# Optimization experiments

Hardware: AMD Instinct MI355X
Metric: run time of the kernel (lower is better)

## Reference

```python
import jax, jax.numpy as jnp
import numpy as np

HIDDEN = 1024
FFN = 2048
NUM_EXPERTS = 8
TOP_K = 2
BATCH = 1
SEQ = 2048


def setup_inputs() -> dict:
    key = jax.random.key(0)
    ks = jax.random.split(key, 5)
    x = jax.random.normal(ks[0], (BATCH, SEQ, HIDDEN), dtype=jnp.float32)
    gate_w = jax.random.normal(ks[1], (NUM_EXPERTS, HIDDEN), dtype=jnp.float32) * 0.02
    w1 = jax.random.normal(ks[2], (NUM_EXPERTS, FFN, HIDDEN), dtype=jnp.float32) * 0.02
    w3 = jax.random.normal(ks[3], (NUM_EXPERTS, FFN, HIDDEN), dtype=jnp.float32) * 0.02
    w2 = jax.random.normal(ks[4], (NUM_EXPERTS, HIDDEN, FFN), dtype=jnp.float32) * 0.02
    return {"x": x, "gate_w": gate_w, "w1": w1, "w3": w3, "w2": w2}


def reference(x, gate_w, w1, w3, w2):
    B, S, H = x.shape
    tokens = x.reshape(-1, H)                              # [T, H]
    # Router: softmax over expert logits, top-k, renormalize (eval mode: no jitter)
    logits = tokens @ gate_w.T                             # [T, E]
    probs = jax.nn.softmax(logits, axis=-1)
    top_w, top_i = jax.lax.top_k(probs, TOP_K)             # [T, K]
    top_w = top_w / jnp.sum(top_w, axis=-1, keepdims=True)
    # combine[t, e] = routing weight of expert e for token t (0 if not selected)
    combine = jnp.sum(
        jax.nn.one_hot(top_i, NUM_EXPERTS, dtype=tokens.dtype) * top_w[..., None],
        axis=1,
    )                                                      # [T, E]
    out = jnp.zeros_like(tokens)
    for e in range(NUM_EXPERTS):
        h = jax.nn.silu(tokens @ w1[e].T) * (tokens @ w3[e].T)   # [T, F]
        out = out + combine[:, e:e + 1] * (h @ w2[e].T)          # [T, H]
    return out.reshape(B, S, H)
```

## Files before the change

kernel.cpp:

```cpp
#include <hip/hip_runtime.h>
#include <hip/hip_bf16.h>

#define T_TOK 2048
#define HID 1024
#define FFNDIM 2048
#define NEXP 8

typedef __attribute__((ext_vector_type(8))) short short8;
typedef __attribute__((ext_vector_type(4))) float f32x4;

__device__ inline unsigned short f2bf(float f) {
  union { float f; unsigned int u; } v; v.f = f;
  unsigned int u = v.u;
  unsigned int r = (u + 0x7fffu + ((u >> 16) & 1u)) >> 16;
  return (unsigned short)r;
}

__device__ inline short8 pack8(float4 a, float4 b) {
  union { __hip_bfloat162 h2[4]; short8 s; } u;
  u.h2[0] = __float22bfloat162_rn(float2{a.x, a.y});
  u.h2[1] = __float22bfloat162_rn(float2{a.z, a.w});
  u.h2[2] = __float22bfloat162_rn(float2{b.x, b.y});
  u.h2[3] = __float22bfloat162_rn(float2{b.z, b.w});
  return u.s;
}

__device__ inline void gload_lds16(const void* g, void* l) {
  __builtin_amdgcn_global_load_lds((const __attribute__((address_space(1))) void*)g,
                                   (__attribute__((address_space(3))) void*)l, 16, 0, 0);
}

__global__ __launch_bounds__(256) void router_kernel(
    const float* __restrict__ x, const float* __restrict__ gw,
    int* __restrict__ top_i, float* __restrict__ top_w,
    unsigned short* __restrict__ xbf) {
  int lane = threadIdx.x & 63;
  int t = blockIdx.x * 4 + (threadIdx.x >> 6);
  if (t >= T_TOK) return;
  float xv[16];
#pragma unroll
  for (int i = 0; i < 16; ++i) xv[i] = x[(size_t)t * HID + i * 64 + lane];
#pragma unroll
  for (int i = 0; i < 16; ++i) xbf[(size_t)t * HID + i * 64 + lane] = f2bf(xv[i]);
  float logit[NEXP];
#pragma unroll
  for (int e = 0; e < NEXP; ++e) {
    float s = 0.f;
#pragma unroll
    for (int i = 0; i < 16; ++i) s += xv[i] * gw[e * HID + i * 64 + lane];
#pragma unroll
    for (int off = 32; off > 0; off >>= 1) s += __shfl_xor(s, off);
    logit[e] = s;
  }
  if (lane == 0) {
    float mx = logit[0];
#pragma unroll
    for (int e = 1; e < NEXP; ++e) mx = fmaxf(mx, logit[e]);
    float p[NEXP]; float sum = 0.f;
#pragma unroll
    for (int e = 0; e < NEXP; ++e) { p[e] = expf(logit[e] - mx); sum += p[e]; }
#pragma unroll
    for (int e = 0; e < NEXP; ++e) p[e] /= sum;
    int i0 = 0;
#pragma unroll
    for (int e = 1; e < NEXP; ++e) if (p[e] > p[i0]) i0 = e;
    int i1 = (i0 == 0) ? 1 : 0;
#pragma unroll
    for (int e = 0; e < NEXP; ++e) if (e != i0 && p[e] > p[i1]) i1 = e;
    float w0 = p[i0], w1v = p[i1];
    float s2 = w0 + w1v;
    w0 /= s2; w1v /= s2;
    top_i[t * 2 + 0] = i0; top_i[t * 2 + 1] = i1;
    top_w[t * 2 + 0] = w0; top_w[t * 2 + 1] = w1v;
  }
}

__global__ __launch_bounds__(256) void plan_kernel(
    const int* __restrict__ top_i, int* __restrict__ counts,
    int* __restrict__ offsets, int* __restrict__ row_tok,
    int* __restrict__ tok_rows) {
  __shared__ int scnt[NEXP], soff[NEXP], scur[NEXP];
  int tid = threadIdx.x;
  if (tid < NEXP) { scnt[tid] = 0; scur[tid] = 0; }
  __syncthreads();
  for (int i = tid; i < T_TOK * 2; i += 256) atomicAdd(&scnt[top_i[i]], 1);
  __syncthreads();
  if (tid == 0) {
    int s = 0;
    for (int e = 0; e < NEXP; ++e) { soff[e] = s; s += scnt[e]; }
  }
  __syncthreads();
  for (int i = tid; i < T_TOK * 2; i += 256) {
    int e = top_i[i];
    int p = atomicAdd(&scur[e], 1);
    int idx = soff[e] + p;
    row_tok[idx] = i >> 1;
    tok_rows[i] = idx;
  }
  if (tid < NEXP) { counts[tid] = scnt[tid]; offsets[tid] = soff[tid]; }
  if (tid == 0) offsets[NEXP] = T_TOK * 2;
}

__global__ __launch_bounds__(256) void wconv_kernel(
    const float4* __restrict__ s0, const float4* __restrict__ s1,
    const float4* __restrict__ s2,
    short8* __restrict__ d0, short8* __restrict__ d1, short8* __restrict__ d2) {
  const float4* s = (blockIdx.y == 0) ? s0 : (blockIdx.y == 1) ? s1 : s2;
  short8* d = (blockIdx.y == 0) ? d0 : (blockIdx.y == 1) ? d1 : d2;
  const int n8 = NEXP * FFNDIM * HID / 8;
  for (int i = blockIdx.x * 256 + threadIdx.x; i < n8; i += gridDim.x * 256) {
    float4 a = s[2 * i];
    float4 b = s[2 * i + 1];
    d[i] = pack8(a, b);
  }
}

__global__ __launch_bounds__(512, 2) void gemm1_s(
    const unsigned short* __restrict__ xbf, const int* __restrict__ row_tok,
    const unsigned short* __restrict__ Wb1, const unsigned short* __restrict__ Wb3,
    const int* __restrict__ counts, const int* __restrict__ offsets,
    unsigned short* __restrict__ hbuf) {
  constexpr int BK = 64;
  constexpr int ATILE = 128 * BK;
  constexpr int BTILE = 256 * BK;
  extern __shared__ unsigned short sm1[];
  unsigned short* sA = sm1;
  unsigned short* sB = sm1 + 2 * ATILE;

  int e = blockIdx.y;
  int cnt = counts[e];
  int nt = blockIdx.x, mt = blockIdx.z;
  if (cnt == 0 || mt * 128 >= cnt) return;
  int off = offsets[e];
  int ntb = nt * 128;

  int tid = threadIdx.x, lane = tid & 63, wid = tid >> 6;
  int wm = wid >> 2, wn = wid & 3;
  int fr = lane & 15, fq = lane >> 4;

  int ri = tid >> 3;
  int g = tid & 7;
  int gsw = (g ^ (ri & 7)) * 8;

  size_t asrc[2]; int albase[2];
#pragma unroll
  for (int j = 0; j < 2; ++j) {
    int r = j * 64 + ri;
    int rg = mt * 128 + r; if (rg > cnt - 1) rg = cnt - 1;
    int tok = row_tok[off + rg];
    asrc[j] = (size_t)tok * HID + gsw;
    albase[j] = (j * 64 + wid * 8) * BK;
  }
  const unsigned short* bsrc[4]; int blbase[4];
#pragma unroll
  for (int j = 0; j < 4; ++j) {
    int r = j * 64 + ri;
    int wn_ = r >> 6, s = r & 63;
    const unsigned short* mat = (s < 32) ? Wb1 : Wb3;
    bsrc[j] = mat + ((size_t)e * FFNDIM + (ntb + wn_ * 32 + (s & 31))) * HID + gsw;
    blbase[j] = (j * 64 + wid * 8) * BK;
  }

#define STAGE1(P, K0)                                                       \
  do {                                                                      \
    _Pragma("unroll")                                                       \
    for (int j = 0; j < 2; ++j)                                             \
      gload_lds16(xbf + asrc[j] + (K0), &sA[(P) * ATILE + albase[j]]);      \
    _Pragma("unroll")                                                       \
    for (int j = 0; j < 4; ++j)                                             \
      gload_lds16(bsrc[j] + (K0), &sB[(P) * BTILE + blbase[j]]);            \
  } while (0)

  f32x4 acc[4][4];
#pragma unroll
  for (int mf = 0; mf < 4; ++mf)
#pragma unroll
    for (int nf = 0; nf < 4; ++nf) acc[mf][nf] = (f32x4){0.f, 0.f, 0.f, 0.f};

#define COMP1(P)                                                            \
  do {                                                                      \
    _Pragma("unroll")                                                       \
    for (int kk = 0; kk < 2; ++kk) {                                        \
      short8 bfr[4];                                                        \
      _Pragma("unroll")                                                     \
      for (int nf = 0; nf < 4; ++nf) {                                      \
        int R = wn * 64 + nf * 16 + fr;                                     \
        bfr[nf] = *reinterpret_cast<const short8*>(                         \
            &sB[(P) * BTILE + R * BK + (((kk * 4 + fq) ^ (R & 7)) << 3)]);  \
      }                                                                     \
      _Pragma("unroll")                                                     \
      for (int mf = 0; mf < 4; ++mf) {                                      \
        int R = wm * 64 + mf * 16 + fr;                                     \
        short8 afr = *reinterpret_cast<const short8*>(                      \
            &sA[(P) * ATILE + R * BK + (((kk * 4 + fq) ^ (R & 7)) << 3)]);  \
        _Pragma("unroll")                                                   \
        for (int nf = 0; nf < 4; ++nf)                                      \
          acc[mf][nf] = __builtin_amdgcn_mfma_f32_16x16x32_bf16(            \
              afr, bfr[nf], acc[mf][nf], 0, 0, 0);                          \
      }                                                                     \
    }                                                                       \
  } while (0)

  const int NT = HID / BK;
  STAGE1(0, 0);
  __syncthreads();
  int cur = 0;
  for (int t = 0; t < NT; ++t) {
    if (t + 1 < NT) STAGE1(cur ^ 1, (t + 1) * BK);
    COMP1(cur);
    __syncthreads();
    cur ^= 1;
  }

#pragma unroll
  for (int mf = 0; mf < 4; ++mf) {
    int rl = wm * 64 + mf * 16 + fq * 4;
#pragma unroll
    for (int jj = 0; jj < 4; ++jj) {
      int gm = mt * 128 + rl + jj;
      if (gm < cnt) {
#pragma unroll
        for (int nf = 0; nf < 2; ++nf) {
          float h1 = acc[mf][nf][jj];
          float h3 = acc[mf][nf + 2][jj];
          float sv = h1 / (1.f + expf(-h1)) * h3;
          hbuf[(size_t)(off + gm) * FFNDIM + ntb + wn * 32 + nf * 16 + fr] = f2bf(sv);
        }
      }
    }
  }
#undef STAGE1
#undef COMP1
}

__global__ __launch_bounds__(512, 2) void gemm2_p(
    const unsigned short* __restrict__ hbuf, const unsigned short* __restrict__ Wb2,
    const int* __restrict__ counts, const int* __restrict__ offsets,
    float* __restrict__ Yg) {
  constexpr int BK = 64;
  constexpr int ATILE = 256 * BK;
  constexpr int BTILE = 128 * BK;
  extern __shared__ unsigned short sm2[];
  unsigned short* sA = sm2;
  unsigned short* sB = sm2 + 2 * ATILE;

  int zz = blockIdx.y;
  int e = zz & 7, kz = zz >> 3;
  int cnt = counts[e];
  int nt = blockIdx.x, mt = blockIdx.z;
  if (cnt == 0 || mt * 256 >= cnt) return;
  int off = offsets[e];
  int ntb = nt * 128;
  int kbase = kz * (FFNDIM / 2);

  int tid = threadIdx.x, lane = tid & 63, wid = tid >> 6;
  int wm = wid >> 2, wn = wid & 3;
  int fr = lane & 15, fq = lane >> 4;

  int ri = tid >> 3;
  int g = tid & 7;
  int gsw = (g ^ (ri & 7)) * 8;

  size_t asrc[4];
  int albase[4];
#pragma unroll
  for (int j = 0; j < 4; ++j) {
    int r = j * 64 + ri;
    int rg = mt * 256 + r; if (rg > cnt - 1) rg = cnt - 1;
    asrc[j] = (size_t)(off + rg) * FFNDIM + kbase + gsw;
    albase[j] = (j * 64 + wid * 8) * BK;
  }
  const unsigned short* bsrc[2];
  int blbase[2];
#pragma unroll
  for (int j = 0; j < 2; ++j) {
    int r = j * 64 + ri;
    bsrc[j] = Wb2 + ((size_t)e * HID + (ntb + r)) * FFNDIM + kbase + gsw;
    blbase[j] = (j * 64 + wid * 8) * BK;
  }

#define STAGE2(P, K0)                                                       \
  do {                                                                      \
    _Pragma("unroll")                                                       \
    for (int j = 0; j < 4; ++j)                                             \
      gload_lds16(hbuf + asrc[j] + (K0), &sA[(P) * ATILE + albase[j]]);     \
    _Pragma("unroll")                                                       \
    for (int j = 0; j < 2; ++j)                                             \
      gload_lds16(bsrc[j] + (K0), &sB[(P) * BTILE + blbase[j]]);            \
  } while (0)

  f32x4 acc[8][2];
#pragma unroll
  for (int mf = 0; mf < 8; ++mf)
#pragma unroll
    for (int nf = 0; nf < 2; ++nf) acc[mf][nf] = (f32x4){0.f, 0.f, 0.f, 0.f};

#define COMP2(P)                                                            \
  do {                                                                      \
    _Pragma("unroll")                                                       \
    for (int kk = 0; kk < 2; ++kk) {                                        \
      short8 bfr[2];                                                        \
      _Pragma("unroll")                                                     \
      for (int nf = 0; nf < 2; ++nf) {                                      \
        int R = wn * 32 + nf * 16 + fr;                                     \
        bfr[nf] = *reinterpret_cast<const short8*>(                         \
            &sB[(P) * BTILE + R * BK + (((kk * 4 + fq) ^ (R & 7)) << 3)]);  \
      }                                                                     \
      _Pragma("unroll")                                                     \
      for (int mf = 0; mf < 8; ++mf) {                                      \
        int R = wm * 128 + mf * 16 + fr;                                    \
        short8 afr = *reinterpret_cast<const short8*>(                      \
            &sA[(P) * ATILE + R * BK + (((kk * 4 + fq) ^ (R & 7)) << 3)]);  \
        _Pragma("unroll")                                                   \
        for (int nf = 0; nf < 2; ++nf)                                      \
          acc[mf][nf] = __builtin_amdgcn_mfma_f32_16x16x32_bf16(            \
              afr, bfr[nf], acc[mf][nf], 0, 0, 0);                          \
      }                                                                     \
    }                                                                       \
  } while (0)

  const int NT = (FFNDIM / 2) / BK;
  STAGE2(0, 0);
  __syncthreads();
  int cur = 0;
  for (int t = 0; t < NT; ++t) {
    if (t + 1 < NT) STAGE2(cur ^ 1, (t + 1) * BK);
    COMP2(cur);
    __syncthreads();
    cur ^= 1;
  }

  float* yp = Yg + (size_t)kz * (4096 * HID);
#pragma unroll
  for (int mf = 0; mf < 8; ++mf) {
    int rl = wm * 128 + mf * 16 + fq * 4;
#pragma unroll
    for (int jj = 0; jj < 4; ++jj) {
      int gm = mt * 256 + rl + jj;
      if (gm < cnt) {
#pragma unroll
        for (int nf = 0; nf < 2; ++nf)
          yp[(size_t)(off + gm) * HID + ntb + wn * 32 + nf * 16 + fr] = acc[mf][nf][jj];
      }
    }
  }
#undef STAGE2
#undef COMP2
}

__global__ __launch_bounds__(256) void combine_kernel(
    const float* __restrict__ Yg, const int* __restrict__ tok_rows,
    const float* __restrict__ top_w, float* __restrict__ out) {
  int t = blockIdx.x;
  int c = threadIdx.x * 4;
  int r0 = tok_rows[t * 2 + 0];
  int r1 = tok_rows[t * 2 + 1];
  float tw0 = top_w[t * 2 + 0];
  float tw1 = top_w[t * 2 + 1];
  const float* Y0 = Yg;
  const float* Y1 = Yg + (size_t)4096 * HID;
  float4 a0 = *reinterpret_cast<const float4*>(Y0 + (size_t)r0 * HID + c);
  float4 b0 = *reinterpret_cast<const float4*>(Y1 + (size_t)r0 * HID + c);
  float4 a1 = *reinterpret_cast<const float4*>(Y0 + (size_t)r1 * HID + c);
  float4 b1 = *reinterpret_cast<const float4*>(Y1 + (size_t)r1 * HID + c);
  float4 o;
  o.x = tw0 * (a0.x + b0.x) + tw1 * (a1.x + b1.x);
  o.y = tw0 * (a0.y + b0.y) + tw1 * (a1.y + b1.y);
  o.z = tw0 * (a0.z + b0.z) + tw1 * (a1.z + b1.z);
  o.w = tw0 * (a0.w + b0.w) + tw1 * (a1.w + b1.w);
  *reinterpret_cast<float4*>(out + (size_t)t * HID + c) = o;
}

extern "C" void kernel_launch(void* const* d_in, const int* in_sizes, int n_in,
                              void* d_out, int out_size, void* d_ws, size_t ws_size,
                              hipStream_t stream) {
  const float* x  = (const float*)d_in[0];
  const float* gw = (const float*)d_in[1];
  const float* w1 = (const float*)d_in[2];
  const float* w3 = (const float*)d_in[3];
  const float* w2 = (const float*)d_in[4];
  float* out = (float*)d_out;

  char* ws = (char*)d_ws;
  int*   counts   = (int*)(ws + 0);
  int*   offsets  = (int*)(ws + 64);
  int*   top_i    = (int*)(ws + 1024);
  float* top_w    = (float*)(ws + 17408);
  int*   row_tok  = (int*)(ws + 33792);
  int*   tok_rows = (int*)(ws + 50176);
  unsigned short* xbf  = (unsigned short*)(ws + 1048576);
  unsigned short* hbuf = (unsigned short*)(ws + 5242880);
  unsigned short* Wb1  = (unsigned short*)(ws + 22020096);
  unsigned short* Wb3  = (unsigned short*)(ws + 55574528);
  unsigned short* Wb2  = (unsigned short*)(ws + 89128960);
  float*          Yg   = (float*)(ws + 22020096);

  hipFuncSetAttribute((const void*)gemm1_s,
                      hipFuncAttributeMaxDynamicSharedMemorySize, 98304);
  hipFuncSetAttribute((const void*)gemm2_p,
                      hipFuncAttributeMaxDynamicSharedMemorySize, 98304);

  router_kernel<<<T_TOK / 4, 256, 0, stream>>>(x, gw, top_i, top_w, xbf);
  plan_kernel<<<1, 256, 0, stream>>>(top_i, counts, offsets, row_tok, tok_rows);
  wconv_kernel<<<dim3(2048, 3), 256, 0, stream>>>(
      (const float4*)w1, (const float4*)w3, (const float4*)w2,
      (short8*)Wb1, (short8*)Wb3, (short8*)Wb2);

  gemm1_s<<<dim3(16, NEXP, 16), 512, 98304, stream>>>(
      xbf, row_tok, Wb1, Wb3, counts, offsets, hbuf);
  gemm2_p<<<dim3(8, 16, 8), 512, 98304, stream>>>(
      hbuf, Wb2, counts, offsets, Yg);
  combine_kernel<<<T_TOK, 256, 0, stream>>>(Yg, tok_rows, top_w, out);
}
```

Measured before the change: 178.0 us.

## Triple-buffer LDS in both expert GEMMs with raw barriers and partial vmcnt waits

Both expert GEMM kernels move from double-buffered to triple-buffered LDS tiles. Loads are issued two K-steps ahead, and each step waits with a partial s_waitcnt vmcnt plus a raw s_barrier instead of a full __syncthreads, so global-to-LDS copies can overlap compute more deeply. The cost is 144KB of shared memory per block, which drops occupancy from 2 blocks per CU to 1 and changes the launch-bounds hint.

New measurement: 175.2 us. Within noise of the previous version (-1.6%).

```diff
diff --git a/kernel.cpp b/kernel.cpp
--- a/kernel.cpp
+++ b/kernel.cpp
@@ -29,6 +29,9 @@
   __builtin_amdgcn_global_load_lds((const __attribute__((address_space(1))) void*)g,
                                    (__attribute__((address_space(3))) void*)l, 16, 0, 0);
 }
+
+#define RAW_BAR() __builtin_amdgcn_s_barrier()
+#define MEMCLOB() asm volatile("" ::: "memory")
 
 __global__ __launch_bounds__(256) void router_kernel(
     const float* __restrict__ x, const float* __restrict__ gw,
@@ -115,7 +118,7 @@
   }
 }
 
-__global__ __launch_bounds__(512, 2) void gemm1_s(
+__global__ __launch_bounds__(512, 1) void gemm1_r3(
     const unsigned short* __restrict__ xbf, const int* __restrict__ row_tok,
     const unsigned short* __restrict__ Wb1, const unsigned short* __restrict__ Wb3,
     const int* __restrict__ counts, const int* __restrict__ offsets,
@@ -125,7 +128,7 @@
   constexpr int BTILE = 256 * BK;
   extern __shared__ unsigned short sm1[];
   unsigned short* sA = sm1;
-  unsigned short* sB = sm1 + 2 * ATILE;
+  unsigned short* sB = sm1 + 3 * ATILE;
 
   int e = blockIdx.y;
   int cnt = counts[e];
@@ -161,14 +164,14 @@
     blbase[j] = (j * 64 + wid * 8) * BK;
   }
 
-#define STAGE1(P, K0)                                                       \
+#define STAGE1(B, K0)                                                       \
   do {                                                                      \
     _Pragma("unroll")                                                       \
     for (int j = 0; j < 2; ++j)                                             \
-      gload_lds16(xbf + asrc[j] + (K0), &sA[(P) * ATILE + albase[j]]);      \
+      gload_lds16(xbf + asrc[j] + (K0), &sA[(B) * ATILE + albase[j]]);      \
     _Pragma("unroll")                                                       \
     for (int j = 0; j < 4; ++j)                                             \
-      gload_lds16(bsrc[j] + (K0), &sB[(P) * BTILE + blbase[j]]);            \
+      gload_lds16(bsrc[j] + (K0), &sB[(B) * BTILE + blbase[j]]);            \
   } while (0)
 
   f32x4 acc[4][4];
@@ -177,7 +180,7 @@
 #pragma unroll
     for (int nf = 0; nf < 4; ++nf) acc[mf][nf] = (f32x4){0.f, 0.f, 0.f, 0.f};
 
-#define COMP1(P)                                                            \
+#define COMP1(B)                                                            \
   do {                                                                      \
     _Pragma("unroll")                                                       \
     for (int kk = 0; kk < 2; ++kk) {                                        \
@@ -186,13 +189,13 @@
       for (int nf = 0; nf < 4; ++nf) {                                      \
         int R = wn * 64 + nf * 16 + fr;                                     \
         bfr[nf] = *reinterpret_cast<const short8*>(                         \
-            &sB[(P) * BTILE + R * BK + (((kk * 4 + fq) ^ (R & 7)) << 3)]);  \
+            &sB[(B) * BTILE + R * BK + (((kk * 4 + fq) ^ (R & 7)) << 3)]);  \
       }                                                                     \
       _Pragma("unroll")                                                     \
       for (int mf = 0; mf < 4; ++mf) {                                      \
         int R = wm * 64 + mf * 16 + fr;                                     \
         short8 afr = *reinterpret_cast<const short8*>(                      \
-            &sA[(P) * ATILE + R * BK + (((kk * 4 + fq) ^ (R & 7)) << 3)]);  \
+            &sA[(B) * ATILE + R * BK + (((kk * 4 + fq) ^ (R & 7)) << 3)]);  \
         _Pragma("unroll")                                                   \
         for (int nf = 0; nf < 4; ++nf)                                      \
           acc[mf][nf] = __builtin_amdgcn_mfma_f32_16x16x32_bf16(            \
@@ -203,13 +206,21 @@
 
   const int NT = HID / BK;
   STAGE1(0, 0);
-  __syncthreads();
-  int cur = 0;
+  STAGE1(1, BK);
+  asm volatile("s_waitcnt vmcnt(6)" ::: "memory");
+  RAW_BAR(); MEMCLOB();
+
+  int bc = 0;
   for (int t = 0; t < NT; ++t) {
-    if (t + 1 < NT) STAGE1(cur ^ 1, (t + 1) * BK);
-    COMP1(cur);
-    __syncthreads();
-    cur ^= 1;
+    int bs = bc + 2; if (bs >= 3) bs -= 3;
+    if (t + 2 < NT) STAGE1(bs, (t + 2) * BK);
+    COMP1(bc);
+    if (t + 1 < NT) {
+      if (t + 2 < NT) asm volatile("s_waitcnt vmcnt(6)" ::: "memory");
+      else            asm volatile("s_waitcnt vmcnt(0)" ::: "memory");
+      RAW_BAR(); MEMCLOB();
+    }
+    ++bc; if (bc >= 3) bc -= 3;
   }
 
 #pragma unroll
@@ -233,7 +244,7 @@
 #undef COMP1
 }
 
-__global__ __launch_bounds__(512, 2) void gemm2_p(
+__global__ __launch_bounds__(512, 1) void gemm2_r3(
     const unsigned short* __restrict__ hbuf, const unsigned short* __restrict__ Wb2,
     const int* __restrict__ counts, const int* __restrict__ offsets,
     float* __restrict__ Yg) {
@@ -242,7 +253,7 @@
   constexpr int BTILE = 128 * BK;
   extern __shared__ unsigned short sm2[];
   unsigned short* sA = sm2;
-  unsigned short* sB = sm2 + 2 * ATILE;
+  unsigned short* sB = sm2 + 3 * ATILE;
 
   int zz = blockIdx.y;
   int e = zz & 7, kz = zz >> 3;
@@ -279,14 +290,14 @@
     blbase[j] = (j * 64 + wid * 8) * BK;
   }
 
-#define STAGE2(P, K0)                                                       \
+#define STAGE2(B, K0)                                                       \
   do {                                                                      \
     _Pragma("unroll")                                                       \
     for (int j = 0; j < 4; ++j)                                             \
-      gload_lds16(hbuf + asrc[j] + (K0), &sA[(P) * ATILE + albase[j]]);     \
+      gload_lds16(hbuf + asrc[j] + (K0), &sA[(B) * ATILE + albase[j]]);     \
     _Pragma("unroll")                                                       \
     for (int j = 0; j < 2; ++j)                                             \
-      gload_lds16(bsrc[j] + (K0), &sB[(P) * BTILE + blbase[j]]);            \
+      gload_lds16(bsrc[j] + (K0), &sB[(B) * BTILE + blbase[j]]);            \
   } while (0)
 
   f32x4 acc[8][2];
@@ -295,7 +306,7 @@
 #pragma unroll
     for (int nf = 0; nf < 2; ++nf) acc[mf][nf] = (f32x4){0.f, 0.f, 0.f, 0.f};
 
-#define COMP2(P)                                                            \
+#define COMP2(B)                                                            \
   do {                                                                      \
     _Pragma("unroll")                                                       \
     for (int kk = 0; kk < 2; ++kk) {                                        \
@@ -304,13 +315,13 @@
       for (int nf = 0; nf < 2; ++nf) {                                      \
         int R = wn * 32 + nf * 16 + fr;                                     \
         bfr[nf] = *reinterpret_cast<const short8*>(                         \
-            &sB[(P) * BTILE + R * BK + (((kk * 4 + fq) ^ (R & 7)) << 3)]);  \
+            &sB[(B) * BTILE + R * BK + (((kk * 4 + fq) ^ (R & 7)) << 3)]);  \
       }                                                                     \
       _Pragma("unroll")                                                     \
       for (int mf = 0; mf < 8; ++mf) {                                      \
         int R = wm * 128 + mf * 16 + fr;                                    \
         short8 afr = *reinterpret_cast<const short8*>(                      \
-            &sA[(P) * ATILE + R * BK + (((kk * 4 + fq) ^ (R & 7)) << 3)]);  \
+            &sA[(B) * ATILE + R * BK + (((kk * 4 + fq) ^ (R & 7)) << 3)]);  \
         _Pragma("unroll")                                                   \
         for (int nf = 0; nf < 2; ++nf)                                      \
           acc[mf][nf] = __builtin_amdgcn_mfma_f32_16x16x32_bf16(            \
@@ -321,13 +332,21 @@
 
   const int NT = (FFNDIM / 2) / BK;
   STAGE2(0, 0);
-  __syncthreads();
-  int cur = 0;
+  STAGE2(1, BK);
+  asm volatile("s_waitcnt vmcnt(6)" ::: "memory");
+  RAW_BAR(); MEMCLOB();
+
+  int bc = 0;
   for (int t = 0; t < NT; ++t) {
-    if (t + 1 < NT) STAGE2(cur ^ 1, (t + 1) * BK);
-    COMP2(cur);
-    __syncthreads();
-    cur ^= 1;
+    int bs = bc + 2; if (bs >= 3) bs -= 3;
+    if (t + 2 < NT) STAGE2(bs, (t + 2) * BK);
+    COMP2(bc);
+    if (t + 1 < NT) {
+      if (t + 2 < NT) asm volatile("s_waitcnt vmcnt(6)" ::: "memory");
+      else            asm volatile("s_waitcnt vmcnt(0)" ::: "memory");
+      RAW_BAR(); MEMCLOB();
+    }
+    ++bc; if (bc >= 3) bc -= 3;
   }
 
   float* yp = Yg + (size_t)kz * (4096 * HID);
@@ -395,10 +414,10 @@
   unsigned short* Wb2  = (unsigned short*)(ws + 89128960);
   float*          Yg   = (float*)(ws + 22020096);
 
-  hipFuncSetAttribute((const void*)gemm1_s,
-                      hipFuncAttributeMaxDynamicSharedMemorySize, 98304);
-  hipFuncSetAttribute((const void*)gemm2_p,
-                      hipFuncAttributeMaxDynamicSharedMemorySize, 98304);
+  hipFuncSetAttribute((const void*)gemm1_r3,
+                      hipFuncAttributeMaxDynamicSharedMemorySize, 147456);
+  hipFuncSetAttribute((const void*)gemm2_r3,
+                      hipFuncAttributeMaxDynamicSharedMemorySize, 147456);
 
   router_kernel<<<T_TOK / 4, 256, 0, stream>>>(x, gw, top_i, top_w, xbf);
   plan_kernel<<<1, 256, 0, stream>>>(top_i, counts, offsets, row_tok, tok_rows);
@@ -406,9 +425,9 @@
       (const float4*)w1, (const float4*)w3, (const float4*)w2,
       (short8*)Wb1, (short8*)Wb3, (short8*)Wb2);
 
-  gemm1_s<<<dim3(16, NEXP, 16), 512, 98304, stream>>>(
+  gemm1_r3<<<dim3(16, NEXP, 16), 512, 147456, stream>>>(
       xbf, row_tok, Wb1, Wb3, counts, offsets, hbuf);
-  gemm2_p<<<dim3(8, 16, 8), 512, 98304, stream>>>(
+  gemm2_r3<<<dim3(8, 16, 8), 512, 147456, stream>>>(
       hbuf, Wb2, counts, offsets, Yg);
   combine_kernel<<<T_TOK, 256, 0, stream>>>(Yg, tok_rows, top_w, out);
 }
```
